# Optimization experiments

Hardware: AMD Instinct MI355X
Metric: run time of the kernel (lower is better)

The kernel has to match this reference:

```python
import jax, jax.numpy as jnp
import numpy as np

N = 50000   # nodes
E = 600000  # edges
D = 128     # in_feats = n_hidden
B = 16384   # pair batch
L = 2       # n_layers
C = 2       # n_classes
EPS = 1e-5


def setup_inputs() -> dict:
    key = jax.random.key(0)
    ks = jax.random.split(key, 16)
    s = 0.05
    return {
        "h": jax.random.normal(ks[0], (N, D), jnp.float32),
        "edge_src": jax.random.randint(ks[1], (E,), 0, N),
        "edge_dst": jax.random.randint(ks[2], (E,), 0, N),
        "x1": jax.random.randint(ks[3], (B,), 0, N),
        "x2": jax.random.randint(ks[4], (B,), 0, N),
        "x1_tar": jax.random.randint(ks[5], (B,), 0, N),
        "x2_tar": jax.random.randint(ks[6], (B,), 0, N),
        # SAGEConv params (mean aggregator): rst = h@W_self + mean_neigh@W_neigh + b
        "W_self": jax.random.normal(ks[7], (L, D, D), jnp.float32) * s,
        "W_neigh": jax.random.normal(ks[8], (L, D, D), jnp.float32) * s,
        "b_conv": jnp.zeros((L, D), jnp.float32),
        # head: linear1(3D->D) -> BN -> relu -> linear2(D->C)
        "W1": jax.random.normal(ks[9], (3 * D, D), jnp.float32) * s,
        "b1": jnp.zeros((D,), jnp.float32),
        "gamma": jnp.ones((D,), jnp.float32),
        "beta": jnp.zeros((D,), jnp.float32),
        "W2": jax.random.normal(ks[10], (D, C), jnp.float32) * s,
        "b2": jnp.zeros((C,), jnp.float32),
    }


def _sage_layers(h, edge_src, edge_dst, W_self, W_neigh, b_conv):
    # in-degree for mean aggregation (clamped to 1 to avoid div by 0)
    deg = jax.ops.segment_sum(jnp.ones((E,), h.dtype), edge_dst, num_segments=N)
    deg = jnp.maximum(deg, 1.0)[:, None]
    for l in range(L):
        msg = h[edge_src]                                        # [E, D] gather
        agg = jax.ops.segment_sum(msg, edge_dst, num_segments=N) / deg  # [N, D]
        h = jax.nn.relu(h @ W_self[l] + agg @ W_neigh[l] + b_conv[l])
    return h


def _pair_feat(h, a, b):
    ha, hb = h[a], h[b]
    return jnp.concatenate([ha, hb, jnp.abs(ha - hb)], axis=1)  # [B, 3D]


def _batchnorm(x, gamma, beta):
    m = x.mean(axis=0)
    v = x.var(axis=0)  # biased variance, as torch BN in training mode normalization
    return (x - m) * jax.lax.rsqrt(v + EPS) * gamma + beta


def reference(h, edge_src, edge_dst, x1, x2, x1_tar, x2_tar,
              W_self, W_neigh, b_conv, W1, b1, gamma, beta, W2, b2):
    h = _sage_layers(h, edge_src, edge_dst, W_self, W_neigh, b_conv)
    h_src = _pair_feat(h, x1, x2) @ W1 + b1
    h_tar = _pair_feat(h, x1_tar, x2_tar) @ W1 + b1
    h_src = _batchnorm(h_src, gamma, beta)
    h_tar = _batchnorm(h_tar, gamma, beta)
    h_src_mmd = jax.nn.relu(h_src)
    h_tar_mmd = jax.nn.relu(h_tar)
    h_p = h_src_mmd @ W2 + b2
    return (h_p, h_src_mmd, h_tar_mmd)
```

## Files before the change

### kernel.cpp

```cpp
#include <hip/hip_runtime.h>

#define NN 50000
#define NE 600000
#define DF 128
#define NB 16384

typedef short bf16x8 __attribute__((ext_vector_type(8)));
typedef float f32x4 __attribute__((ext_vector_type(4)));

__device__ __forceinline__ float bf2f(unsigned short u){
  return __uint_as_float(((unsigned int)u) << 16);
}
__device__ __forceinline__ unsigned short f2bf(float x){
  unsigned int b = __float_as_uint(x);
  return (unsigned short)((b + 0x7FFFu + ((b >> 16) & 1u)) >> 16);
}

__global__ void GraphSAGE_8504035246140_kernel(){ }

__global__ __launch_bounds__(256) void k_prelude(
    const float* h_in, unsigned short* h_c,
    const float* Ws, const float* Wn, const float* W1,
    unsigned short* WsB, unsigned short* WnB, unsigned short* W1B,
    int* cnt, float* stats){
  int b = blockIdx.x, t = threadIdx.x;
  if (b < 3125){
    int i = b * 256 + t;
    const float4* s = (const float4*)h_in;
    float4 v0 = s[i * 2], v1 = s[i * 2 + 1];
    unsigned short d[8] = {f2bf(v0.x), f2bf(v0.y), f2bf(v0.z), f2bf(v0.w),
                           f2bf(v1.x), f2bf(v1.y), f2bf(v1.z), f2bf(v1.w)};
    *(bf16x8*)(h_c + i * 8) = *(bf16x8*)d;
  } else if (b < 3516){
    int i = (b - 3125) * 256 + t;
    if (i < 2 * NN) cnt[i] = 0;
  } else if (b < 3518){
    int i = (b - 3516) * 256 + t;
    if (i < 512) stats[i] = 0.f;
  } else {
    int idx = (b - 3518) * 256 + t;
    if (idx < 2 * DF * DF){
      int layer = idx >> 14;
      int e = idx & (DF * DF - 1);
      int k = e >> 7, n = e & 127;
      int dst = layer * DF * DF + (((k >> 3) * 128 + n) << 3) + (k & 7);
      WsB[dst] = f2bf(Ws[idx]);
      WnB[dst] = f2bf(Wn[idx]);
    }
    if (idx < 3 * DF * DF){
      int k = idx >> 7, n = idx & 127;
      W1B[(((k >> 3) * 128 + n) << 3) + (k & 7)] = f2bf(W1[idx]);
    }
  }
}

__global__ void k_hist(const int* dst, int* cnt){
  int e = blockIdx.x * 256 + threadIdx.x;
  if (e < NE) atomicAdd(&cnt[dst[e]], 1);
}
__global__ void k_scan1(const int* cnt, int* bsum){
  __shared__ int l[256];
  int t = threadIdx.x, i = blockIdx.x * 256 + t;
  l[t] = (i < NN) ? cnt[i] : 0;
  __syncthreads();
  for (int o = 128; o > 0; o >>= 1){
    if (t < o) l[t] += l[t + o];
    __syncthreads();
  }
  if (t == 0) bsum[blockIdx.x] = l[0];
}
__global__ void k_scan3(const int* cnt, const int* bsum, int* rp){
  __shared__ int bs[256];
  __shared__ int l[256];
  int t = threadIdx.x, i = blockIdx.x * 256 + t;
  bs[t] = (t < 196) ? bsum[t] : 0;
  int v = (i < NN) ? cnt[i] : 0;
  l[t] = v;
  __syncthreads();
  for (int o = 1; o < 256; o <<= 1){
    int xb = (t >= o) ? bs[t - o] : 0;
    int xl = (t >= o) ? l[t - o] : 0;
    __syncthreads();
    bs[t] += xb; l[t] += xl;
    __syncthreads();
  }
  int base = (blockIdx.x == 0) ? 0 : bs[blockIdx.x - 1];
  if (i < NN){
    rp[i] = base + l[t] - v;
    if (i == NN - 1) rp[NN] = base + l[t];
  }
}
__global__ void k_scatter(const int* src, const int* dst,
                          const int* rp, int* fill, int* perm){
  int e = blockIdx.x * 256 + threadIdx.x;
  if (e < NE){
    int d = dst[e];
    int pos = atomicAdd(&fill[d], 1);
    perm[rp[d] + pos] = src[e];
  }
}

__global__ __launch_bounds__(256) void k_agg(
    const unsigned int* hb32, const int* rp, const int* perm,
    unsigned int* agg32){
  int n = blockIdx.x * 4 + (threadIdx.x >> 6);
  if (n >= NN) return;
  int l = threadIdx.x & 63;
  int rs = l >> 4, li = l & 15;
  int s = rp[n], e = rp[n + 1];
  const unsigned int* hq = hb32 + li * 4;
  float a0 = 0.f, a1 = 0.f, a2 = 0.f, a3 = 0.f;
  float a4 = 0.f, a5 = 0.f, a6 = 0.f, a7 = 0.f;
  int i = s;
  for (; i + 16 <= e; i += 16){
    int p0 = perm[i + rs];
    int p1 = perm[i + 4 + rs];
    int p2 = perm[i + 8 + rs];
    int p3 = perm[i + 12 + rs];
    uint4 x0 = *(const uint4*)(hq + (size_t)p0 * 64);
    uint4 x1 = *(const uint4*)(hq + (size_t)p1 * 64);
    uint4 x2 = *(const uint4*)(hq + (size_t)p2 * 64);
    uint4 x3 = *(const uint4*)(hq + (size_t)p3 * 64);
    a0 += __uint_as_float(x0.x << 16); a1 += __uint_as_float(x0.x & 0xffff0000u);
    a2 += __uint_as_float(x0.y << 16); a3 += __uint_as_float(x0.y & 0xffff0000u);
    a4 += __uint_as_float(x0.z << 16); a5 += __uint_as_float(x0.z & 0xffff0000u);
    a6 += __uint_as_float(x0.w << 16); a7 += __uint_as_float(x0.w & 0xffff0000u);
    a0 += __uint_as_float(x1.x << 16); a1 += __uint_as_float(x1.x & 0xffff0000u);
    a2 += __uint_as_float(x1.y << 16); a3 += __uint_as_float(x1.y & 0xffff0000u);
    a4 += __uint_as_float(x1.z << 16); a5 += __uint_as_float(x1.z & 0xffff0000u);
    a6 += __uint_as_float(x1.w << 16); a7 += __uint_as_float(x1.w & 0xffff0000u);
    a0 += __uint_as_float(x2.x << 16); a1 += __uint_as_float(x2.x & 0xffff0000u);
    a2 += __uint_as_float(x2.y << 16); a3 += __uint_as_float(x2.y & 0xffff0000u);
    a4 += __uint_as_float(x2.z << 16); a5 += __uint_as_float(x2.z & 0xffff0000u);
    a6 += __uint_as_float(x2.w << 16); a7 += __uint_as_float(x2.w & 0xffff0000u);
    a0 += __uint_as_float(x3.x << 16); a1 += __uint_as_float(x3.x & 0xffff0000u);
    a2 += __uint_as_float(x3.y << 16); a3 += __uint_as_float(x3.y & 0xffff0000u);
    a4 += __uint_as_float(x3.z << 16); a5 += __uint_as_float(x3.z & 0xffff0000u);
    a6 += __uint_as_float(x3.w << 16); a7 += __uint_as_float(x3.w & 0xffff0000u);
  }
  if (i < e){
    int i0 = i + rs, i1 = i + 4 + rs, i2 = i + 8 + rs, i3 = i + 12 + rs;
    int p0 = perm[i0 < e ? i0 : s];
    int p1 = perm[i1 < e ? i1 : s];
    int p2 = perm[i2 < e ? i2 : s];
    int p3 = perm[i3 < e ? i3 : s];
    uint4 x0 = *(const uint4*)(hq + (size_t)p0 * 64);
    uint4 x1 = *(const uint4*)(hq + (size_t)p1 * 64);
    uint4 x2 = *(const uint4*)(hq + (size_t)p2 * 64);
    uint4 x3 = *(const uint4*)(hq + (size_t)p3 * 64);
    if (i0 < e){
      a0 += __uint_as_float(x0.x << 16); a1 += __uint_as_float(x0.x & 0xffff0000u);
      a2 += __uint_as_float(x0.y << 16); a3 += __uint_as_float(x0.y & 0xffff0000u);
      a4 += __uint_as_float(x0.z << 16); a5 += __uint_as_float(x0.z & 0xffff0000u);
      a6 += __uint_as_float(x0.w << 16); a7 += __uint_as_float(x0.w & 0xffff0000u);
    }
    if (i1 < e){
      a0 += __uint_as_float(x1.x << 16); a1 += __uint_as_float(x1.x & 0xffff0000u);
      a2 += __uint_as_float(x1.y << 16); a3 += __uint_as_float(x1.y & 0xffff0000u);
      a4 += __uint_as_float(x1.z << 16); a5 += __uint_as_float(x1.z & 0xffff0000u);
      a6 += __uint_as_float(x1.w << 16); a7 += __uint_as_float(x1.w & 0xffff0000u);
    }
    if (i2 < e){
      a0 += __uint_as_float(x2.x << 16); a1 += __uint_as_float(x2.x & 0xffff0000u);
      a2 += __uint_as_float(x2.y << 16); a3 += __uint_as_float(x2.y & 0xffff0000u);
      a4 += __uint_as_float(x2.z << 16); a5 += __uint_as_float(x2.z & 0xffff0000u);
      a6 += __uint_as_float(x2.w << 16); a7 += __uint_as_float(x2.w & 0xffff0000u);
    }
    if (i3 < e){
      a0 += __uint_as_float(x3.x << 16); a1 += __uint_as_float(x3.x & 0xffff0000u);
      a2 += __uint_as_float(x3.y << 16); a3 += __uint_as_float(x3.y & 0xffff0000u);
      a4 += __uint_as_float(x3.z << 16); a5 += __uint_as_float(x3.z & 0xffff0000u);
      a6 += __uint_as_float(x3.w << 16); a7 += __uint_as_float(x3.w & 0xffff0000u);
    }
  }
  a0 += __shfl_xor(a0, 16); a1 += __shfl_xor(a1, 16);
  a2 += __shfl_xor(a2, 16); a3 += __shfl_xor(a3, 16);
  a4 += __shfl_xor(a4, 16); a5 += __shfl_xor(a5, 16);
  a6 += __shfl_xor(a6, 16); a7 += __shfl_xor(a7, 16);
  a0 += __shfl_xor(a0, 32); a1 += __shfl_xor(a1, 32);
  a2 += __shfl_xor(a2, 32); a3 += __shfl_xor(a3, 32);
  a4 += __shfl_xor(a4, 32); a5 += __shfl_xor(a5, 32);
  a6 += __shfl_xor(a6, 32); a7 += __shfl_xor(a7, 32);
  if (rs == 0){
    float di = 1.0f / fmaxf((float)(e - s), 1.0f);
    uint4 r;
    r.x = (unsigned int)f2bf(a0 * di) | ((unsigned int)f2bf(a1 * di) << 16);
    r.y = (unsigned int)f2bf(a2 * di) | ((unsigned int)f2bf(a3 * di) << 16);
    r.z = (unsigned int)f2bf(a4 * di) | ((unsigned int)f2bf(a5 * di) << 16);
    r.w = (unsigned int)f2bf(a6 * di) | ((unsigned int)f2bf(a7 * di) << 16);
    *(uint4*)(agg32 + (size_t)n * 64 + li * 4) = r;
  }
}

__global__ __launch_bounds__(256) void k_layer_mfma(
    const unsigned short* hb, const unsigned short* aggb,
    const unsigned short* WsB, const unsigned short* WnB,
    const float* bias, unsigned short* hout){
  int t = threadIdx.x;
  int w = t >> 6, l = t & 63;
  int m = l & 15, q = l >> 4;
  int r0 = blockIdx.x * 128 + w * 16;
  int arow0 = r0 + m;       if (arow0 > NN - 1) arow0 = NN - 1;
  int arow1 = r0 + 64 + m;  if (arow1 > NN - 1) arow1 = NN - 1;
  const unsigned short* hp0 = hb   + (size_t)arow0 * DF + q * 8;
  const unsigned short* ap0 = aggb + (size_t)arow0 * DF + q * 8;
  const unsigned short* hp1 = hb   + (size_t)arow1 * DF + q * 8;
  const unsigned short* ap1 = aggb + (size_t)arow1 * DF + q * 8;
  f32x4 acc0[8], acc1[8];
  for (int ct = 0; ct < 8; ++ct){
    float bbc = bias[ct * 16 + m];
    acc0[ct] = (f32x4){bbc, bbc, bbc, bbc};
    acc1[ct] = (f32x4){bbc, bbc, bbc, bbc};
  }
  for (int kt = 0; kt < 4; ++kt){
    bf16x8 a_h0 = *(const bf16x8*)(hp0 + kt * 32);
    bf16x8 a_g0 = *(const bf16x8*)(ap0 + kt * 32);
    bf16x8 a_h1 = *(const bf16x8*)(hp1 + kt * 32);
    bf16x8 a_g1 = *(const bf16x8*)(ap1 + kt * 32);
    int kg = kt * 4 + q;
    for (int ct = 0; ct < 8; ++ct){
      bf16x8 b_s = *(const bf16x8*)(WsB + (((kg << 7) + ct * 16 + m) << 3));
      bf16x8 b_n = *(const bf16x8*)(WnB + (((kg << 7) + ct * 16 + m) << 3));
      acc0[ct] = __builtin_amdgcn_mfma_f32_16x16x32_bf16(a_h0, b_s, acc0[ct], 0, 0, 0);
      acc0[ct] = __builtin_amdgcn_mfma_f32_16x16x32_bf16(a_g0, b_n, acc0[ct], 0, 0, 0);
      acc1[ct] = __builtin_amdgcn_mfma_f32_16x16x32_bf16(a_h1, b_s, acc1[ct], 0, 0, 0);
      acc1[ct] = __builtin_amdgcn_mfma_f32_16x16x32_bf16(a_g1, b_n, acc1[ct], 0, 0, 0);
    }
  }
  for (int ct = 0; ct < 8; ++ct){
    int col = ct * 16 + m;
    for (int reg = 0; reg < 4; ++reg){
      int row0 = r0 + q * 4 + reg;
      int row1 = row0 + 64;
      if (row0 < NN) hout[(size_t)row0 * DF + col] = f2bf(fmaxf(acc0[ct][reg], 0.f));
      if (row1 < NN) hout[(size_t)row1 * DF + col] = f2bf(fmaxf(acc1[ct][reg], 0.f));
    }
  }
}

__global__ __launch_bounds__(256) void k_pair_mfma(
    const unsigned short* h2,
    const int* x1, const int* x2, const int* x1t, const int* x2t,
    const unsigned short* W1B, const float* b1, float* zbase, float* stats){
  __shared__ __align__(16) unsigned short F[64 * 392];
  __shared__ float csum[128], csq[128];
  int g = blockIdx.y;
  const int* ia = g ? x1t : x1;
  const int* ib = g ? x2t : x2;
  float* z = zbase + (size_t)g * NB * DF;
  int t = threadIdx.x;
  if (t < 128){ csum[t] = 0.f; csq[t] = 0.f; }
  int r0 = blockIdx.x * 64;
  int i = t >> 2, qq = t & 3;
  int r = r0 + i;
  int a = ia[r], b = ib[r];
  const unsigned short* pa = h2 + (size_t)a * DF + qq * 32;
  const unsigned short* pb = h2 + (size_t)b * DF + qq * 32;
  unsigned short* fr = F + i * 392;
  for (int jj = 0; jj < 4; ++jj){
    bf16x8 va = *(const bf16x8*)(pa + jj * 8);
    bf16x8 vb = *(const bf16x8*)(pb + jj * 8);
    *(bf16x8*)(fr + qq * 32 + jj * 8) = va;
    *(bf16x8*)(fr + 128 + qq * 32 + jj * 8) = vb;
    unsigned short d[8];
    for (int e = 0; e < 8; ++e){
      float fa = bf2f((unsigned short)va[e]);
      float fb = bf2f((unsigned short)vb[e]);
      d[e] = f2bf(fabsf(fa - fb));
    }
    *(bf16x8*)(fr + 256 + qq * 32 + jj * 8) = *(bf16x8*)d;
  }
  __syncthreads();
  int w = t >> 6, l = t & 63;
  int m = l & 15, q = l >> 4;
  int rl = w * 16 + m;
  f32x4 acc[8];
  for (int ct = 0; ct < 8; ++ct){
    float bbc = b1[ct * 16 + m];
    acc[ct] = (f32x4){bbc, bbc, bbc, bbc};
  }
  for (int kt = 0; kt < 12; ++kt){
    bf16x8 af = *(const bf16x8*)(F + rl * 392 + kt * 32 + q * 8);
    int kg = kt * 4 + q;
    for (int ct = 0; ct < 8; ++ct){
      bf16x8 bfr = *(const bf16x8*)(W1B + (((kg << 7) + ct * 16 + m) << 3));
      acc[ct] = __builtin_amdgcn_mfma_f32_16x16x32_bf16(af, bfr, acc[ct], 0, 0, 0);
    }
  }
  for (int ct = 0; ct < 8; ++ct){
    int col = ct * 16 + m;
    int row = r0 + w * 16 + q * 4;
    float s = 0.f, s2 = 0.f;
    for (int reg = 0; reg < 4; ++reg){
      float v = acc[ct][reg];
      z[(size_t)(row + reg) * DF + col] = v;
      s += v; s2 += v * v;
    }
    atomicAdd(&csum[col], s);
    atomicAdd(&csq[col], s2);
  }
  __syncthreads();
  if (t < 128){
    atomicAdd(&stats[g * 256 + t], csum[t]);
    atomicAdd(&stats[g * 256 + 128 + t], csq[t]);
  }
}

__global__ __launch_bounds__(256) void k_norm_hp(
    const float* zbase, const float* stats,
    const float* gamma, const float* beta,
    const float* W2, const float* b2, float* mmd_base, float* hp){
  int g = blockIdx.y;
  int t = threadIdx.x;
  int w = t >> 6, l = t & 63;
  int c0 = l * 2, c1 = c0 + 1;
  float m0 = stats[g * 256 + c0] * (1.0f / NB);
  float m1 = stats[g * 256 + c1] * (1.0f / NB);
  float v0 = stats[g * 256 + 128 + c0] * (1.0f / NB) - m0 * m0;
  float v1 = stats[g * 256 + 128 + c1] * (1.0f / NB) - m1 * m1;
  float is0 = 1.0f / sqrtf(v0 + 1e-5f);
  float is1 = 1.0f / sqrtf(v1 + 1e-5f);
  float ga0 = gamma[c0], ga1 = gamma[c1];
  float be0 = beta[c0], be1 = beta[c1];
  float w200 = W2[c0 * 2], w201 = W2[c0 * 2 + 1];
  float w210 = W2[c1 * 2], w211 = W2[c1 * 2 + 1];
  const float* z = zbase + (size_t)g * NB * DF;
  float* mmd = mmd_base + (size_t)g * NB * DF;
  int rbase = blockIdx.x * 16 + w * 4;
  for (int rr = 0; rr < 4; ++rr){
    int row = rbase + rr;
    float2 zv = *(const float2*)(z + (size_t)row * DF + c0);
    float y0 = fmaxf((zv.x - m0) * is0 * ga0 + be0, 0.f);
    float y1 = fmaxf((zv.y - m1) * is1 * ga1 + be1, 0.f);
    float2 yv; yv.x = y0; yv.y = y1;
    *(float2*)(mmd + (size_t)row * DF + c0) = yv;
    if (g == 0){
      float s0 = y0 * w200 + y1 * w210;
      float s1 = y0 * w201 + y1 * w211;
      for (int o = 32; o > 0; o >>= 1){
        s0 += __shfl_xor(s0, o);
        s1 += __shfl_xor(s1, o);
      }
      if (l == 0){
        hp[row * 2]     = s0 + b2[0];
        hp[row * 2 + 1] = s1 + b2[1];
      }
    }
  }
}

extern "C" __attribute__((used, visibility("default")))
void kernel_launch(void* const* d_in, const int* in_sizes, int n_in,
                   void* d_out, int out_size, void* d_ws, size_t ws_size,
                   hipStream_t stream){
  const float* h_in  = (const float*)d_in[0];
  const int* esrc = (const int*)d_in[1];
  const int* edst = (const int*)d_in[2];
  const int* x1   = (const int*)d_in[3];
  const int* x2   = (const int*)d_in[4];
  const int* x1t  = (const int*)d_in[5];
  const int* x2t  = (const int*)d_in[6];
  const float* Wself = (const float*)d_in[7];
  const float* Wneigh= (const float*)d_in[8];
  const float* bconv = (const float*)d_in[9];
  const float* W1    = (const float*)d_in[10];
  const float* b1    = (const float*)d_in[11];
  const float* gamma = (const float*)d_in[12];
  const float* beta  = (const float*)d_in[13];
  const float* W2    = (const float*)d_in[14];
  const float* b2    = (const float*)d_in[15];
  float* out = (float*)d_out;
  float* hp_out   = out;
  float* mmd_base = out + 2 * NB;

  float* zreg  = (float*)d_ws;
  unsigned short* aggb = (unsigned short*)zreg;
  float* stats = zreg + (size_t)2 * NB * DF;
  float* mstd  = stats + 512;
  float* dinv  = mstd + 512;
  int* cnt  = (int*)(dinv + 50048);
  int* fill = cnt + NN;
  int* rp   = fill + NN;
  int* perm = rp + 50016;
  int* bsum = perm + 600000;
  unsigned short* h_c = (unsigned short*)(bsum + 256);
  unsigned short* h1b = h_c + (size_t)NN * DF;
  unsigned short* h2b = h_c;
  unsigned short* WsB = h1b + (size_t)NN * DF;
  unsigned short* WnB = WsB + 2 * DF * DF;
  unsigned short* W1B = WnB + 2 * DF * DF;
  (void)dinv;

  k_prelude<<<3710, 256, 0, stream>>>(h_in, h_c, Wself, Wneigh, W1,
                                      WsB, WnB, W1B, cnt, stats);

  k_hist<<<(NE + 255) / 256, 256, 0, stream>>>(edst, cnt);
  k_scan1<<<196, 256, 0, stream>>>(cnt, bsum);
  k_scan3<<<196, 256, 0, stream>>>(cnt, bsum, rp);
  k_scatter<<<(NE + 255) / 256, 256, 0, stream>>>(esrc, edst, rp, fill, perm);

  k_agg<<<(NN + 3) / 4, 256, 0, stream>>>((const unsigned int*)h_c, rp, perm,
                                          (unsigned int*)aggb);
  k_layer_mfma<<<(NN + 127) / 128, 256, 0, stream>>>(h_c, aggb, WsB, WnB,
                                                     bconv, h1b);
  k_agg<<<(NN + 3) / 4, 256, 0, stream>>>((const unsigned int*)h1b, rp, perm,
                                          (unsigned int*)aggb);
  k_layer_mfma<<<(NN + 127) / 128, 256, 0, stream>>>(h1b, aggb, WsB + DF * DF,
                                                     WnB + DF * DF, bconv + DF,
                                                     h2b);

  k_pair_mfma<<<dim3(NB / 64, 2), 256, 0, stream>>>(h2b, x1, x2, x1t, x2t,
                                                    W1B, b1, zreg, stats);
  k_norm_hp<<<dim3(NB / 16, 2), 256, 0, stream>>>(zreg, stats, gamma, beta,
                                                  W2, b2, mmd_base, hp_out);
}
```

Baseline: 279.8 us.

## Replace atomic CSR scatter with two-pass bucketed radix scatter in shared memory

New measurement: 285.8 us. +2.2%, slower.

```diff
diff --git a/kernel.cpp b/kernel.cpp
--- a/kernel.cpp
+++ b/kernel.cpp
@@ -4,6 +4,9 @@
 #define NE 600000
 #define DF 128
 #define NB 16384
+#define SCA_B 128
+#define SCA_PER ((NE + SCA_B - 1) / SCA_B)
+#define SCB_CAP 4352
 
 typedef short bf16x8 __attribute__((ext_vector_type(8)));
 typedef float f32x4 __attribute__((ext_vector_type(4)));
@@ -69,7 +72,7 @@
   }
   if (t == 0) bsum[blockIdx.x] = l[0];
 }
-__global__ void k_scan3(const int* cnt, const int* bsum, int* rp){
+__global__ void k_scan3(const int* cnt, const int* bsum, int* rp, int* cfill){
   __shared__ int bs[256];
   __shared__ int l[256];
   int t = threadIdx.x, i = blockIdx.x * 256 + t;
@@ -86,17 +89,90 @@
   }
   int base = (blockIdx.x == 0) ? 0 : bs[blockIdx.x - 1];
   if (i < NN){
-    rp[i] = base + l[t] - v;
+    int r = base + l[t] - v;
+    rp[i] = r;
+    if (t == 0) cfill[blockIdx.x] = r;
     if (i == NN - 1) rp[NN] = base + l[t];
   }
 }
-__global__ void k_scatter(const int* src, const int* dst,
-                          const int* rp, int* fill, int* perm){
-  int e = blockIdx.x * 256 + threadIdx.x;
-  if (e < NE){
+
+__global__ __launch_bounds__(256) void k_scatA(
+    const int* src, const int* dst, int* cfill, unsigned int* tmp){
+  __shared__ unsigned int hist[196];
+  __shared__ unsigned int bstart[197];
+  __shared__ int gbase[196];
+  __shared__ unsigned int buf[SCA_PER];
+  int t = threadIdx.x;
+  int e0 = blockIdx.x * SCA_PER;
+  int e1 = e0 + SCA_PER; if (e1 > NE) e1 = NE;
+  for (int i = t; i < 196; i += 256) hist[i] = 0;
+  __syncthreads();
+  for (int e = e0 + t; e < e1; e += 256) atomicAdd(&hist[dst[e] >> 8], 1u);
+  __syncthreads();
+  if (t == 0){
+    unsigned int acc = 0;
+    for (int b = 0; b < 196; ++b){ bstart[b] = acc; acc += hist[b]; }
+    bstart[196] = acc;
+  }
+  __syncthreads();
+  for (int b = t; b < 196; b += 256){
+    gbase[b] = atomicAdd(&cfill[b], (int)hist[b]);
+    hist[b] = bstart[b];
+  }
+  __syncthreads();
+  for (int e = e0 + t; e < e1; e += 256){
     int d = dst[e];
-    int pos = atomicAdd(&fill[d], 1);
-    perm[rp[d] + pos] = src[e];
+    unsigned int off = atomicAdd(&hist[d >> 8], 1u);
+    buf[off] = (unsigned int)src[e] | ((unsigned int)(d & 255) << 16);
+  }
+  __syncthreads();
+  int total = e1 - e0;
+  for (int j = t; j < total; j += 256){
+    int lo = 0, hi = 195;
+    while (lo < hi){ int mid = (lo + hi + 1) >> 1;
+      if ((int)bstart[mid] <= j) lo = mid; else hi = mid - 1; }
+    tmp[gbase[lo] + (j - (int)bstart[lo])] = buf[j];
+  }
+}
+
+__global__ __launch_bounds__(256) void k_scatB(
+    const unsigned int* tmp, const int* rp, int* fill, int* perm){
+  __shared__ unsigned int hist[256];
+  __shared__ unsigned int ebuf[SCB_CAP];
+  __shared__ unsigned int sbuf[SCB_CAP];
+  int b = blockIdx.x, t = threadIdx.x;
+  int n0 = b << 8;
+  int n1 = n0 + 256; if (n1 > NN) n1 = NN;
+  int s = rp[n0], e = rp[n1];
+  int cntb = e - s;
+  if (cntb <= SCB_CAP){
+    for (int i = t; i < 256; i += 256) hist[i] = 0;
+    __syncthreads();
+    for (int i = t; i < cntb; i += 256){
+      unsigned int v = tmp[s + i];
+      ebuf[i] = v;
+      atomicAdd(&hist[(v >> 16) & 255], 1u);
+    }
+    __syncthreads();
+    if (t == 0){
+      unsigned int acc = 0;
+      for (int k = 0; k < 256; ++k){ unsigned int c = hist[k]; hist[k] = acc; acc += c; }
+    }
+    __syncthreads();
+    for (int i = t; i < cntb; i += 256){
+      unsigned int v = ebuf[i];
+      unsigned int off = atomicAdd(&hist[(v >> 16) & 255], 1u);
+      sbuf[off] = v;
+    }
+    __syncthreads();
+    for (int i = t; i < cntb; i += 256) perm[s + i] = (int)(sbuf[i] & 0xFFFFu);
+  } else {
+    for (int i = t; i < cntb; i += 256){
+      unsigned int v = tmp[s + i];
+      int node = n0 + (int)((v >> 16) & 255);
+      int pos = atomicAdd(&fill[node], 1);
+      perm[rp[node] + pos] = (int)(v & 0xFFFFu);
+    }
   }
 }
 
@@ -383,12 +459,14 @@
   int* rp   = fill + NN;
   int* perm = rp + 50016;
   int* bsum = perm + 600000;
-  unsigned short* h_c = (unsigned short*)(bsum + 256);
+  int* cfill = bsum + 256;
+  unsigned short* h_c = (unsigned short*)(cfill + 256);
   unsigned short* h1b = h_c + (size_t)NN * DF;
   unsigned short* h2b = h_c;
   unsigned short* WsB = h1b + (size_t)NN * DF;
   unsigned short* WnB = WsB + 2 * DF * DF;
   unsigned short* W1B = WnB + 2 * DF * DF;
+  unsigned int* tmp = (unsigned int*)(W1B + 3 * DF * DF);
   (void)dinv;
 
   k_prelude<<<3710, 256, 0, stream>>>(h_in, h_c, Wself, Wneigh, W1,
@@ -396,8 +474,9 @@
 
   k_hist<<<(NE + 255) / 256, 256, 0, stream>>>(edst, cnt);
   k_scan1<<<196, 256, 0, stream>>>(cnt, bsum);
-  k_scan3<<<196, 256, 0, stream>>>(cnt, bsum, rp);
-  k_scatter<<<(NE + 255) / 256, 256, 0, stream>>>(esrc, edst, rp, fill, perm);
+  k_scan3<<<196, 256, 0, stream>>>(cnt, bsum, rp, cfill);
+  k_scatA<<<SCA_B, 256, 0, stream>>>(esrc, edst, cfill, tmp);
+  k_scatB<<<196, 256, 0, stream>>>(tmp, rp, fill, perm);
 
   k_agg<<<(NN + 3) / 4, 256, 0, stream>>>((const unsigned int*)h_c, rp, perm,
                                           (unsigned int*)aggb);
```
